# Optimization experiments

Measured on AMD Instinct MI355X. Metric: run time of the kernel, lower is better.

Reference implementation:

```python
import jax, jax.numpy as jnp
import numpy as np

H = 12      # num_heads
EPS = 1e-5  # LayerNorm eps (torch default)


def _ln(x, g, b):
    m = x.mean(-1, keepdims=True)
    v = x.var(-1, keepdims=True)
    return (x - m) * jax.lax.rsqrt(v + EPS) * g + b


def _rot_half(x):
    x1, x2 = x[..., 0::2], x[..., 1::2]
    return jnp.stack((-x2, x1), axis=-1).reshape(x.shape)


def _rope_tables(n, head_dim):
    # rotary-embedding-torch: RotaryEmbedding(dim=head_dim//2, use_xpos=True),
    # theta=10000, scale_base=512. Only first rot=head_dim//2 dims are rotated.
    rot = head_dim // 2
    inv = 1.0 / (10000.0 ** (jnp.arange(0, rot, 2, dtype=jnp.float32) / rot))
    t = jnp.arange(n, dtype=jnp.float32)
    freqs = jnp.repeat(t[:, None] * inv[None, :], 2, axis=-1)  # (n, rot), interleaved
    base = (jnp.arange(0, rot, 2, dtype=jnp.float32) + 0.4 * rot) / (1.4 * rot)
    power = (t - n // 2) / 512.0
    sc = base[None, :] ** power[:, None]
    sc = jnp.concatenate([sc, sc], axis=-1)  # (n, rot), concatenated (library behavior)
    return jnp.cos(freqs), jnp.sin(freqs), sc


def _attn_path(xn, Wqkv, bqkv, Wproj, bproj, qg, qb, kg, kb, R, rg, rb):
    B, N, D = xn.shape
    d = D // H
    qkv = xn @ Wqkv + bqkv
    q, k, v = jnp.split(qkv, 3, axis=-1)
    hd = lambda t: t.reshape(B, N, H, d).transpose(0, 2, 1, 3)  # (B,H,N,d)
    q, k, v = hd(q), hd(k), hd(v)
    q = _ln(q, qg, qb)  # per-head QK LayerNorm
    k = _ln(k, kg, kb)
    cos, sin, sc = _rope_tables(N, d)
    rot = d // 2

    def rope(t, s):  # rotate only first rot dims
        tl, tr = t[..., :rot], t[..., rot:]
        tl = tl * cos * s + _rot_half(tl) * sin * s
        return jnp.concatenate([tl, tr], axis=-1)

    q = rope(q, sc)
    v = rope(v, 1.0 / sc)  # source applies rope to (q, v), not k

    scores = jnp.einsum('bhid,bhjd->bhij', q, k) / jnp.sqrt(jnp.asarray(d, xn.dtype))
    p = jax.nn.softmax(scores, axis=-1)
    # SDPA(q,k,ones_NN)[...,i,j] == sum_k p[...,i,k] for every j (constant over j).
    # All downstream ops (head-mix einsum, LayerNorm over heads, @ v) therefore
    # reduce exactly to the per-(b,i) computation below, avoiding an N^3 matmul.
    s = p.sum(-1)                              # (B,H,N)
    mix = jnp.einsum('bhi,hg->big', s, R)      # (B,N,H)
    w = _ln(mix, rg, rb)                       # reattn LayerNorm over head axis
    vsum = v.sum(axis=2)                       # (B,H,d); (w @ v) with w const over j
    y = jnp.einsum('big,bgd->bigd', w, vsum).reshape(B, N, D)
    return y @ Wproj + bproj


def _cgmlp(xn, W1, b1, gg, gb, cw, cb, W2, b2):
    h = jax.nn.gelu(xn @ W1 + b1, approximate=False)
    c2 = h.shape[-1] // 2
    xr, xg = h[..., :c2], h[..., c2:]
    xg = _ln(xg, gg, gb).transpose(0, 2, 1)  # (B,C,T)
    K = cw.shape[-1]
    xg = jax.lax.conv_general_dilated(xg, cw, (1,), [((K - 1) // 2, (K - 1) // 2)],
                                      dimension_numbers=('NCH', 'OIH', 'NCH'),
                                      feature_group_count=c2)  # depthwise conv1d
    xg = (xg + cb[None, :, None]).transpose(0, 2, 1)
    return (xr * xg) @ W2 + b2


def reference(x, Wqkv, bqkv, Wproj, bproj, qn_g, qn_b, kn_g, kn_b, reattn_w, rn_g, rn_b,
              ln1_g, ln1_b, ln2_g, ln2_b, ls1, ls2, W1, b1, gn_g, gn_b, conv_w, conv_b,
              W2, b2, Wout, bout):
    # eval mode: dropout / drop_path are identity
    xa = _ln(x, ln1_g, ln1_b)
    attn = sum(_attn_path(xa, Wqkv[p], bqkv[p], Wproj[p], bproj[p], qn_g[p], qn_b[p],
                          kn_g[p], kn_b[p], reattn_w[p], rn_g[p], rn_b[p])
               for p in range(2))
    x_attn = x + ls1 * attn
    xm = _ln(x, ln2_g, ln2_b)
    x_mlp = x + ls2 * _cgmlp(xm, W1, b1, gn_g, gn_b, conv_w, conv_b, W2, b2)
    xf = jnp.concatenate([x_attn, x_mlp], axis=-1)
    return xf @ Wout + bout + x


def setup_inputs():
    B, N, D, P = 4, 1024, 768, 2
    d = D // H
    C = 4 * D
    c2 = C // 2
    K = 21
    ks = iter(jax.random.split(jax.random.key(0), 16))
    nrm = lambda s, sd=0.02: jax.random.normal(next(ks), s, jnp.float32) * sd
    return {
        'x': jax.random.normal(next(ks), (B, N, D), jnp.float32),
        'Wqkv': nrm((P, D, 3 * D)), 'bqkv': jnp.zeros((P, 3 * D)),
        'Wproj': nrm((P, D, D)), 'bproj': jnp.zeros((P, D)),
        'qn_g': jnp.ones((P, d)), 'qn_b': jnp.zeros((P, d)),
        'kn_g': jnp.ones((P, d)), 'kn_b': jnp.zeros((P, d)),
        'reattn_w': jax.random.normal(next(ks), (P, H, H), jnp.float32),
        'rn_g': jnp.ones((P, H)), 'rn_b': jnp.zeros((P, H)),
        'ln1_g': jnp.ones((D,)), 'ln1_b': jnp.zeros((D,)),
        'ln2_g': jnp.ones((D,)), 'ln2_b': jnp.zeros((D,)),
        'ls1': jnp.full((D,), 0.01, jnp.float32), 'ls2': jnp.full((D,), 0.01, jnp.float32),
        'W1': nrm((D, C)), 'b1': jnp.zeros((C,)),
        'gn_g': jnp.ones((c2,)), 'gn_b': jnp.zeros((c2,)),
        'conv_w': nrm((c2, 1, K), 0.1), 'conv_b': jnp.zeros((c2,)),
        'W2': nrm((c2, D)), 'b2': jnp.zeros((D,)),
        'Wout': nrm((2 * D, D)), 'bout': jnp.zeros((D,)),
    }
```

## Files before the change

### kernel.cpp

```cpp
#include <hip/hip_runtime.h>
#include <hip/hip_bf16.h>

typedef short s16x8 __attribute__((ext_vector_type(8)));
typedef float f32x4 __attribute__((ext_vector_type(4)));

#define C2 1536

__device__ __forceinline__ float b2f(ushort u){ return __uint_as_float(((unsigned)u)<<16); }
__device__ __forceinline__ ushort f2b(float f){ unsigned u = __float_as_uint(f); return (ushort)((u + 0x7fffu + ((u>>16)&1u)) >> 16); }

#define GL16(g, l) __builtin_amdgcn_global_load_lds( \
    (const __attribute__((address_space(1))) void*)(g), \
    (__attribute__((address_space(3))) void*)(l), 16, 0, 0)

#define VMW(n) asm volatile("s_waitcnt vmcnt(" #n ")" ::: "memory")
#define LGW()  asm volatile("s_waitcnt lgkmcnt(0)" ::: "memory")
#define SB()   __builtin_amdgcn_sched_barrier(0)
#define BAR()  __builtin_amdgcn_s_barrier()
#define SP1    __builtin_amdgcn_s_setprio(1)
#define SP0    __builtin_amdgcn_s_setprio(0)
#define MF(va, vb, c) __builtin_amdgcn_mfma_f32_16x16x32_bf16(va, vb, c, 0,0,0)

#define RDA(P, mh) { const int ab = (P) + aro + (mh)*4096; \
    a0=L8(ab+sx0);      a1=L8(ab+sx1); \
    a2=L8(ab+1024+sx0); a3=L8(ab+1024+sx1); \
    a4=L8(ab+2048+sx0); a5=L8(ab+2048+sx1); \
    a6=L8(ab+3072+sx0); a7=L8(ab+3072+sx1); }
#define RDB0(P, nh) { const int bb = (P) + bro + (nh)*2048; \
    b00=L8(bb+sx0); b01=L8(bb+sx1); b02=L8(bb+1024+sx0); b03=L8(bb+1024+sx1); }
#define RDB1(P, nh) { const int bb = (P) + bro + (nh)*2048; \
    b10=L8(bb+sx0); b11=L8(bb+sx1); b12=L8(bb+1024+sx0); b13=L8(bb+1024+sx1); }
#define L8(off) (*(const s16x8*)&lds[off])
#define STG(p0, p1, T, dstb) { \
    GL16((p0) + (size_t)(T)*64, &lds[(dstb) + ldsw]); \
    GL16((p1) + (size_t)(T)*64, &lds[(dstb) + 4096 + ldsw]); }
#define QD(mh, nh, B0,B1,B2,B3) { \
  acc[(mh)*4+0][(nh)*2+0]=MF(a0,B0,acc[(mh)*4+0][(nh)*2+0]); \
  acc[(mh)*4+0][(nh)*2+0]=MF(a1,B1,acc[(mh)*4+0][(nh)*2+0]); \
  acc[(mh)*4+0][(nh)*2+1]=MF(a0,B2,acc[(mh)*4+0][(nh)*2+1]); \
  acc[(mh)*4+0][(nh)*2+1]=MF(a1,B3,acc[(mh)*4+0][(nh)*2+1]); \
  acc[(mh)*4+1][(nh)*2+0]=MF(a2,B0,acc[(mh)*4+1][(nh)*2+0]); \
  acc[(mh)*4+1][(nh)*2+0]=MF(a3,B1,acc[(mh)*4+1][(nh)*2+0]); \
  acc[(mh)*4+1][(nh)*2+1]=MF(a2,B2,acc[(mh)*4+1][(nh)*2+1]); \
  acc[(mh)*4+1][(nh)*2+1]=MF(a3,B3,acc[(mh)*4+1][(nh)*2+1]); \
  acc[(mh)*4+2][(nh)*2+0]=MF(a4,B0,acc[(mh)*4+2][(nh)*2+0]); \
  acc[(mh)*4+2][(nh)*2+0]=MF(a5,B1,acc[(mh)*4+2][(nh)*2+0]); \
  acc[(mh)*4+2][(nh)*2+1]=MF(a4,B2,acc[(mh)*4+2][(nh)*2+1]); \
  acc[(mh)*4+2][(nh)*2+1]=MF(a5,B3,acc[(mh)*4+2][(nh)*2+1]); \
  acc[(mh)*4+3][(nh)*2+0]=MF(a6,B0,acc[(mh)*4+3][(nh)*2+0]); \
  acc[(mh)*4+3][(nh)*2+0]=MF(a7,B1,acc[(mh)*4+3][(nh)*2+0]); \
  acc[(mh)*4+3][(nh)*2+1]=MF(a6,B2,acc[(mh)*4+3][(nh)*2+1]); \
  acc[(mh)*4+3][(nh)*2+1]=MF(a7,B3,acc[(mh)*4+3][(nh)*2+1]); }

#define EIGHT(t0, t1, DS, VM4) \
   VMW(4); BAR(); \
  RDA(0,0); RDB0(0,0); \
  STG(pA00,pA01,(t1), 16384); \
  LGW(); SB(); SP1; QD(0,0,b00,b01,b02,b03); SP0; BAR(); \
   RDB1(0,1); \
  STG(pA10,pA11,(t1), 24576); \
  BAR(); LGW(); SB(); SP1; QD(0,1,b10,b11,b12,b13); SP0; BAR(); \
   RDA(0,1); \
  if (DS) { STG(pB00,pB01,(t0)+2, 32768); } \
  BAR(); LGW(); SB(); SP1; QD(1,0,b00,b01,b02,b03); SP0; BAR(); \
   if (DS) { STG(pB10,pB11,(t0)+2, 40960); } \
  BAR(); SP1; QD(1,1,b10,b11,b12,b13); SP0; BAR(); \
   VM4; BAR(); \
  RDA(16384,0); RDB0(16384,0); \
  if (DS) { STG(pA00,pA01,(t0)+2, 0); } \
  LGW(); SB(); SP1; QD(0,0,b00,b01,b02,b03); SP0; BAR(); \
   RDB1(16384,1); \
  if (DS) { STG(pA10,pA11,(t0)+2, 8192); } \
  BAR(); LGW(); SB(); SP1; QD(0,1,b10,b11,b12,b13); SP0; BAR(); \
   RDA(16384,1); \
  if (DS) { STG(pB00,pB01,(t1)+2, 49152); } \
  BAR(); LGW(); SB(); SP1; QD(1,0,b00,b01,b02,b03); SP0; BAR(); \
   if (DS) { STG(pB10,pB11,(t1)+2, 57344); } \
  BAR(); SP1; QD(1,1,b10,b11,b12,b13); SP0; BAR();

template<int EPI>
__global__ __launch_bounds__(512, 1) void gemm256(
    const ushort* __restrict__ A, const ushort* __restrict__ BT,
    int M, int N, int K,
    const float* __restrict__ bias,
    ushort* __restrict__ o16, ushort* __restrict__ o16b)
{
    extern __shared__ ushort lds[];
    const int t = threadIdx.x;
    const int lane = t & 63, wv = t >> 6;
    const int wr = wv >> 2, wc = wv & 3;
    const int r0 = lane & 15, q = lane >> 4, e7 = lane & 7;
    const int m0 = blockIdx.y*256, n0 = blockIdx.x*256;

    const int idx = wv*64 + lane;
    const int lr8 = idx >> 3;
    const int ksrc = (idx & 7) ^ (lr8 & 7);
    const ushort* pA00 = A  + (size_t)(m0 +   0 +  0 + lr8)*K + ksrc*8;
    const ushort* pA01 = A  + (size_t)(m0 +   0 + 64 + lr8)*K + ksrc*8;
    const ushort* pA10 = A  + (size_t)(m0 + 128 +  0 + lr8)*K + ksrc*8;
    const ushort* pA11 = A  + (size_t)(m0 + 128 + 64 + lr8)*K + ksrc*8;
    const ushort* pB00 = BT + (size_t)(n0 +   0 +  0 + lr8)*K + ksrc*8;
    const ushort* pB01 = BT + (size_t)(n0 +   0 + 64 + lr8)*K + ksrc*8;
    const ushort* pB10 = BT + (size_t)(n0 + 128 +  0 + lr8)*K + ksrc*8;
    const ushort* pB11 = BT + (size_t)(n0 + 128 + 64 + lr8)*K + ksrc*8;
    const int ldsw = wv*512;

    const int aro = (wr*128 + r0)*64;
    const int bro = 32768 + (wc*64 + r0)*64;
    const int sx0 = (q ^ e7)*8, sx1 = ((q ^ e7)*8) ^ 32;

    f32x4 acc[8][4];
    #pragma unroll
    for (int i=0;i<8;++i)
        #pragma unroll
        for (int j=0;j<4;++j) acc[i][j] = (f32x4){0.f,0.f,0.f,0.f};
    s16x8 a0,a1,a2,a3,a4,a5,a6,a7;
    s16x8 b00,b01,b02,b03, b10,b11,b12,b13;

    const int nkt = K >> 6;
    const int niter = nkt >> 1;

    STG(pB00,pB01, 0, 32768);
    STG(pB10,pB11, 0, 40960);
    STG(pA00,pA01, 0, 0);
    STG(pA10,pA11, 0, 8192);
    STG(pB00,pB01, 1, 49152);
    STG(pB10,pB11, 1, 57344);

    for (int i = 0; i < niter-1; ++i) {
        const int t0 = 2*i, t1 = 2*i+1;
        EIGHT(t0, t1, 1, VMW(4));
    }
    {
        const int t0 = nkt-2, t1 = nkt-1;
        EIGHT(t0, t1, 0, VMW(0));
    }

    #pragma unroll
    for (int gm=0; gm<8; ++gm) {
        #pragma unroll
        for (int gn=0; gn<4; ++gn) {
            int col = n0 + wc*64 + gn*16 + r0;
            #pragma unroll
            for (int r=0; r<4; ++r) {
                int row = m0 + wr*128 + gm*16 + q*4 + r;
                float v = acc[gm][gn][r];
                if (EPI == 0) {
                    o16[(size_t)row*N + col] = f2b(v + bias[col]);
                } else {
                    v += bias[col];
                    float g = 0.5f*v*(1.0f + erff(v*0.70710678118f));
                    if (col < C2) o16 [(size_t)row*C2 + col]        = f2b(g);
                    else          o16b[(size_t)row*C2 + (col - C2)] = f2b(g);
                }
            }
        }
    }
}

template<int EPI>
__global__ __launch_bounds__(256) void gemm_bf16(
    const ushort* __restrict__ A, const ushort* __restrict__ BT,
    int M, int N, int K, int lda, int ldbt,
    const float* __restrict__ bias, const float* __restrict__ xres,
    ushort* __restrict__ o16, float* __restrict__ o32)
{
    __shared__ ushort Al[2][128*32];
    __shared__ ushort Bl[2][128*32];
    const int t = threadIdx.x;
    const int m0 = blockIdx.y*128, n0 = blockIdx.x*128;
    const int lane = t & 63, wv = t >> 6;
    const int wm = (wv>>1)*64, wn = (wv&1)*64;
    const int r0 = lane & 15, q = lane >> 4;

    const int c0i = t, c1i = t + 256;
    const int lrow0 = ((c0i>>6)<<4) | (c0i&15), lkc0 = ((c0i>>4)&3) << 3;
    const int lrow1 = ((c1i>>6)<<4) | (c1i&15), lkc1 = ((c1i>>4)&3) << 3;
    const ushort* gA0 = A  + (size_t)(m0+lrow0)*lda + lkc0;
    const ushort* gB0 = BT + (size_t)(n0+lrow0)*ldbt + lkc0;
    const ushort* gA1 = A  + (size_t)(m0+lrow1)*lda + lkc1;
    const ushort* gB1 = BT + (size_t)(n0+lrow1)*ldbt + lkc1;

    f32x4 acc[4][4];
    #pragma unroll
    for (int i=0;i<4;++i)
        #pragma unroll
        for (int j=0;j<4;++j) acc[i][j] = (f32x4){0.f,0.f,0.f,0.f};

    const int nkt = K >> 5;
    uint4 pa0_0, pb0_0, pa1_0, pb1_0;
    uint4 pa0_1, pb0_1, pa1_1, pb1_1;
    pa0_0 = *(const uint4*)gA0;        pb0_0 = *(const uint4*)gB0;
    pa1_0 = *(const uint4*)gA1;        pb1_0 = *(const uint4*)gB1;
    pa0_1 = *(const uint4*)(gA0 + 32); pb0_1 = *(const uint4*)(gB0 + 32);
    pa1_1 = *(const uint4*)(gA1 + 32); pb1_1 = *(const uint4*)(gB1 + 32);
    *(uint4*)&Al[0][c0i*8] = pa0_0;
    *(uint4*)&Bl[0][c0i*8] = pb0_0;
    *(uint4*)&Al[0][c1i*8] = pa1_0;
    *(uint4*)&Bl[0][c1i*8] = pb1_0;

    for (int kt = 0; kt < nkt; kt += 2) {
        __syncthreads();
        {
            s16x8 af[4], bfr[4];
            #pragma unroll
            for (int mt=0; mt<4; ++mt) af[mt]  = *(const s16x8*)&Al[0][(((wm>>4)+mt)*64 + lane)*8];
            #pragma unroll
            for (int nt=0; nt<4; ++nt) bfr[nt] = *(const s16x8*)&Bl[0][(((wn>>4)+nt)*64 + lane)*8];
            *(uint4*)&Al[1][c0i*8] = pa0_1;
            *(uint4*)&Bl[1][c0i*8] = pb0_1;
            *(uint4*)&Al[1][c1i*8] = pa1_1;
            *(uint4*)&Bl[1][c1i*8] = pb1_1;
            if (kt+2 < nkt) {
                pa0_0 = *(const uint4*)(gA0 + (kt+2)*32);
                pb0_0 = *(const uint4*)(gB0 + (kt+2)*32);
                pa1_0 = *(const uint4*)(gA1 + (kt+2)*32);
                pb1_0 = *(const uint4*)(gB1 + (kt+2)*32);
            }
            #pragma unroll
            for (int mt=0; mt<4; ++mt)
                #pragma unroll
                for (int nt=0; nt<4; ++nt)
                    acc[mt][nt] = __builtin_amdgcn_mfma_f32_16x16x32_bf16(af[mt], bfr[nt], acc[mt][nt], 0,0,0);
        }
        __syncthreads();
        {
            s16x8 af[4], bfr[4];
            #pragma unroll
            for (int mt=0; mt<4; ++mt) af[mt]  = *(const s16x8*)&Al[1][(((wm>>4)+mt)*64 + lane)*8];
            #pragma unroll
            for (int nt=0; nt<4; ++nt) bfr[nt] = *(const s16x8*)&Bl[1][(((wn>>4)+nt)*64 + lane)*8];
            if (kt+2 < nkt) {
                *(uint4*)&Al[0][c0i*8] = pa0_0;
                *(uint4*)&Bl[0][c0i*8] = pb0_0;
                *(uint4*)&Al[0][c1i*8] = pa1_0;
                *(uint4*)&Bl[0][c1i*8] = pb1_0;
            }
            if (kt+3 < nkt) {
                pa0_1 = *(const uint4*)(gA0 + (kt+3)*32);
                pb0_1 = *(const uint4*)(gB0 + (kt+3)*32);
                pa1_1 = *(const uint4*)(gA1 + (kt+3)*32);
                pb1_1 = *(const uint4*)(gB1 + (kt+3)*32);
            }
            #pragma unroll
            for (int mt=0; mt<4; ++mt)
                #pragma unroll
                for (int nt=0; nt<4; ++nt)
                    acc[mt][nt] = __builtin_amdgcn_mfma_f32_16x16x32_bf16(af[mt], bfr[nt], acc[mt][nt], 0,0,0);
        }
    }

    #pragma unroll
    for (int mt=0; mt<4; ++mt) {
        #pragma unroll
        for (int nt=0; nt<4; ++nt) {
            int col = n0 + wn + nt*16 + r0;
            #pragma unroll
            for (int r=0; r<4; ++r) {
                int row = m0 + wm + mt*16 + q*4 + r;
                float v = acc[mt][nt][r];
                if (EPI == 0) {
                    o16[(size_t)row*N + col] = f2b(v + bias[col]);
                } else if (EPI == 3) {
                    o32[(size_t)row*768 + col] = v + bias[(row>>10)*768 + col] + xres[(size_t)row*768 + col];
                } else {
                    o16[(size_t)row*2304 + 768 + col] = f2b(v);
                }
            }
        }
    }
}

__global__ __launch_bounds__(256) void pack_bt(const float* __restrict__ src, ushort* __restrict__ dst,
                                               int K, int ld, int coff)
{
    __shared__ float tl[32*33];
    int kt = blockIdx.x*32, nt = blockIdx.y*32;
    int nl = threadIdx.x & 31, kg = threadIdx.x >> 5;
    #pragma unroll
    for (int kk=0; kk<4; ++kk) {
        int k = kg*4 + kk;
        tl[k*33 + nl] = src[(size_t)(kt + k)*ld + coff + nt + nl];
    }
    __syncthreads();
    int kcol = threadIdx.x & 31, ng = threadIdx.x >> 5;
    #pragma unroll
    for (int nn=0; nn<4; ++nn) {
        int nrow = ng*4 + nn;
        dst[(size_t)(nt + nrow)*K + kt + kcol] = f2b(tl[kcol*33 + nrow]);
    }
}

__global__ __launch_bounds__(256) void pack_bts(const float* __restrict__ src,
    const float* __restrict__ scale, ushort* __restrict__ dst)
{
    __shared__ float tl[32*33];
    int kt = blockIdx.x*32, nt = blockIdx.y*32;
    int nl = threadIdx.x & 31, kg = threadIdx.x >> 5;
    #pragma unroll
    for (int kk=0; kk<4; ++kk) {
        int k = kg*4 + kk;
        tl[k*33 + nl] = src[(size_t)(kt + k)*768 + nt + nl];
    }
    __syncthreads();
    int kcol = threadIdx.x & 31, ng = threadIdx.x >> 5;
    #pragma unroll
    for (int nn=0; nn<4; ++nn) {
        int nrow = ng*4 + nn;
        dst[(size_t)(nt + nrow)*768 + kt + kcol] = f2b(tl[kcol*33 + nrow] * scale[kt + kcol]);
    }
}

__global__ __launch_bounds__(256) void fold1_pack(const float* __restrict__ Wout, ushort* __restrict__ dst)
{
    __shared__ float tl[32*33];
    int kt = blockIdx.x*32, nt = blockIdx.y*32;
    int nl = threadIdx.x & 31, kg = threadIdx.x >> 5;
    #pragma unroll
    for (int kk=0; kk<4; ++kk) {
        int k = kg*4 + kk;
        tl[k*33 + nl] = Wout[(size_t)(kt + k)*768 + nt + nl]
                      + Wout[(size_t)(768 + kt + k)*768 + nt + nl];
    }
    __syncthreads();
    int kcol = threadIdx.x & 31, ng = threadIdx.x >> 5;
    #pragma unroll
    for (int nn=0; nn<4; ++nn) {
        int nrow = ng*4 + nn;
        dst[(size_t)(nt + nrow)*2304 + kt + kcol] = f2b(tl[kcol*33 + nrow]);
    }
}

__global__ __launch_bounds__(256) void cast16(const float* __restrict__ src, ushort* __restrict__ dst, int n)
{
    int i = blockIdx.x*256 + threadIdx.x;
    if (i < n) dst[i] = f2b(src[i]);
}

__global__ __launch_bounds__(256) void pack_bv(const float* __restrict__ bqkv, float* __restrict__ bvp)
{
    int idx = blockIdx.x*256 + threadIdx.x;
    if (idx < 1536) bvp[idx] = bqkv[(idx/768)*2304 + 1536 + (idx%768)];
}

__global__ __launch_bounds__(256) void cvec_kernel(const float* __restrict__ attn_c,
    const float* __restrict__ ls1, const float* __restrict__ ls2, const float* __restrict__ b2,
    const float* __restrict__ Wout, float* __restrict__ cvecb)
{
    int o  = blockIdx.x*256 + threadIdx.x;
    int r0 = blockIdx.y * 96;
    int b  = blockIdx.z;
    float acc = 0.f;
    #pragma unroll 4
    for (int rr = 0; rr < 96; ++rr) {
        int r = r0 + rr;
        float coef = (r < 768) ? ls1[r]*attn_c[b*768 + r]
                               : ls2[r-768]*b2[r-768];
        acc += coef * Wout[(size_t)r*768 + o];
    }
    atomicAdd(&cvecb[b*768 + o], acc);
}

__global__ __launch_bounds__(256) void ln_x_kernel(const float* __restrict__ x,
    const float* __restrict__ g1, const float* __restrict__ b1,
    const float* __restrict__ g2, const float* __restrict__ b2,
    ushort* __restrict__ xa, ushort* __restrict__ xm, ushort* __restrict__ xc)
{
    __shared__ float sb[8];
    int row = blockIdx.x; int t = threadIdx.x;
    float v[3]; float s = 0.f, ss = 0.f;
    #pragma unroll
    for (int e=0; e<3; ++e) { v[e] = x[(size_t)row*768 + t + e*256]; s += v[e]; ss += v[e]*v[e]; }
    for (int o=32; o>0; o>>=1){ s += __shfl_down(s,o,64); ss += __shfl_down(ss,o,64); }
    int lane = t&63, w = t>>6;
    if (lane==0){ sb[w]=s; sb[4+w]=ss; }
    __syncthreads();
    s = sb[0]+sb[1]+sb[2]+sb[3]; ss = sb[4]+sb[5]+sb[6]+sb[7];
    float mean = s*(1.f/768.f);
    float var  = ss*(1.f/768.f) - mean*mean;
    float rstd = rsqrtf(var + 1e-5f);
    #pragma unroll
    for (int e=0; e<3; ++e){
        int c = t + e*256;
        float n = (v[e]-mean)*rstd;
        xa[(size_t)row*768 + c] = f2b(n*g1[c] + b1[c]);
        xm[(size_t)row*768 + c] = f2b(n*g2[c] + b2[c]);
        xc[(size_t)row*2304 + c] = f2b(v[e]);
    }
}

__global__ __launch_bounds__(256) void prep_kernel(
    float* __restrict__ w1t, float* __restrict__ w2t, float* __restrict__ wvec,
    float* __restrict__ attn_c, float* __restrict__ vsum, float* __restrict__ cvecb,
    const float* __restrict__ R, const float* __restrict__ rng,
    const float* __restrict__ rnb, const float* __restrict__ bproj,
    const float* __restrict__ bout)
{
    int idx = blockIdx.x*256 + threadIdx.x;
    {
        int i = idx >> 6, j = idx & 63;
        float w1, w2;
        if (j < 32) {
            int m = j >> 1;
            float inv = powf(10000.f, -(float)m*(1.f/16.f));
            float fr = (float)i * inv;
            float c = cosf(fr), sn = sinf(fr);
            float power = ((float)i - 512.f) * (1.f/512.f);
            float basev = (2.f*(float)(j & 15) + 12.8f) * (1.f/44.8f);
            float sfac = powf(basev, -power);
            w1 = c * sfac;
            w2 = ((j & 1) ? sn : -sn) * sfac;
        } else { w1 = 1.f; w2 = 0.f; }
        w1t[idx] = w1; w2t[idx] = w2;
    }
    if (blockIdx.x >= 1 && blockIdx.x <= 12) {
        int k = (blockIdx.x-1)*256 + threadIdx.x;
        int o = k % 768;
        attn_c[k] = bproj[o] + bproj[768 + o];
    }
    if (blockIdx.x >= 13 && blockIdx.x <= 36) {
        int k = (blockIdx.x-13)*256 + threadIdx.x;
        vsum[k] = 0.f;
    }
    if (blockIdx.x >= 37 && blockIdx.x <= 48) {
        int k = (blockIdx.x-37)*256 + threadIdx.x;
        cvecb[k] = bout[k % 768];
    }
    if (blockIdx.x == 0) {
        __shared__ float mixs[24];
        __shared__ float ws[24];
        int t = threadIdx.x;
        if (t < 24) {
            int p = t / 12, g = t % 12;
            float m = 0.f;
            for (int h=0; h<12; ++h) m += R[p*144 + h*12 + g];
            mixs[t] = m;
        }
        __syncthreads();
        if (t < 2) {
            float mean=0.f, var=0.f;
            for (int g=0; g<12; ++g) mean += mixs[t*12+g];
            mean *= (1.f/12.f);
            for (int g=0; g<12; ++g){ float d = mixs[t*12+g]-mean; var += d*d; }
            var *= (1.f/12.f);
            float rstd = rsqrtf(var + 1e-5f);
            for (int g=0; g<12; ++g)
                ws[t*12+g] = (mixs[t*12+g]-mean)*rstd*rng[t*12+g] + rnb[t*12+g];
        }
        __syncthreads();
        if (t < 24) wvec[t] = ws[t];
    }
}

__global__ __launch_bounds__(256) void rope_reduce(const ushort* __restrict__ V,
    const float* __restrict__ w1t, const float* __restrict__ w2t, float* __restrict__ vsum)
{
    int col = blockIdx.x*256 + threadIdx.x;
    int b = blockIdx.y;
    int i0 = blockIdx.z * 256;
    int j = col & 63;
    float acc = 0.f;
    const ushort* vp = V + (size_t)(b*1024 + i0)*1536;
    #pragma unroll 4
    for (int i=0; i<256; ++i) {
        float v1 = b2f(vp[(size_t)i*1536 + col]);
        float v2 = b2f(vp[(size_t)i*1536 + (col^1)]);
        int ii = i0 + i;
        acc += w1t[ii*64 + j]*v1 + w2t[ii*64 + j]*v2;
    }
    atomicAdd(&vsum[b*1536 + col], acc);
}

__global__ __launch_bounds__(256) void attn_gemm(const float* __restrict__ vsum,
    const float* __restrict__ wvec, const float* __restrict__ Wproj, float* __restrict__ attn_c)
{
    int o  = blockIdx.x*256 + threadIdx.x;
    int c0 = blockIdx.y * 96;
    int b  = blockIdx.z;
    int p  = c0 / 768;
    float acc = 0.f;
    #pragma unroll 4
    for (int cc=0; cc<96; ++cc) {
        int c = c0 + cc;
        int cl = c - p*768;
        float y = wvec[p*12 + (cl>>6)] * vsum[b*1536 + c];
        acc += y * Wproj[(size_t)p*589824 + (size_t)cl*768 + o];
    }
    atomicAdd(&attn_c[b*768 + o], acc);
}

__global__ __launch_bounds__(256) void ln_gate(const ushort* __restrict__ xg,
    const float* __restrict__ g, const float* __restrict__ bta, ushort* __restrict__ out)
{
    __shared__ float sb[8];
    int row = blockIdx.x, t = threadIdx.x;
    float v[6]; float s=0.f, ss=0.f;
    #pragma unroll
    for (int e=0;e<6;++e){ v[e] = b2f(xg[(size_t)row*1536 + t + e*256]); s+=v[e]; ss+=v[e]*v[e]; }
    for (int o=32; o>0; o>>=1){ s += __shfl_down(s,o,64); ss += __shfl_down(ss,o,64); }
    int lane = t&63, w = t>>6;
    if (lane==0){ sb[w]=s; sb[4+w]=ss; }
    __syncthreads();
    s = sb[0]+sb[1]+sb[2]+sb[3]; ss = sb[4]+sb[5]+sb[6]+sb[7];
    float mean = s*(1.f/1536.f);
    float var  = ss*(1.f/1536.f) - mean*mean;
    float rstd = rsqrtf(var + 1e-5f);
    #pragma unroll
    for (int e=0;e<6;++e){
        int c = t + e*256;
        out[(size_t)row*1536 + c] = f2b((v[e]-mean)*rstd*g[c] + bta[c]);
    }
}

#define CROWS 128
#define CIN   (CROWS + 20)
#define CSTR  72
__global__ __launch_bounds__(256) void conv_mul(const ushort* __restrict__ xgln,
    const float* __restrict__ cw, const float* __restrict__ cb,
    const ushort* __restrict__ xr, ushort* __restrict__ u)
{
    __shared__ ushort tile[CIN * CSTR];
    const int c0 = blockIdx.x * 64;
    const int i0 = blockIdx.y * CROWS;
    const int b  = blockIdx.z;
    const int t  = threadIdx.x;
    const size_t base = (size_t)b*1024*1536;

    #pragma unroll
    for (int it = 0; it < 5; ++it) {
        int idx = it*256 + t;
        if (idx < CIN*8) {
            int r  = idx >> 3;
            int cq = (idx & 7) * 8;
            int si = i0 + r - 10;
            uint4 val = make_uint4(0u,0u,0u,0u);
            if (si >= 0 && si < 1024)
                val = *(const uint4*)(xgln + base + (size_t)si*1536 + c0 + cq);
            *(uint4*)&tile[r*CSTR + cq] = val;
        }
    }
    __syncthreads();

    const int ch = t & 63;
    const int o0 = (t >> 6) * 32;
    const int c  = c0 + ch;

    float w[21];
    #pragma unroll
    for (int k=0; k<21; ++k) w[k] = cw[c*21 + k];
    const float bias = cb[c];

    float win[21];
    #pragma unroll
    for (int j=0; j<20; ++j) win[j] = b2f(tile[(o0+j)*CSTR + ch]);

    #pragma unroll
    for (int j=0; j<32; ++j) {
        win[(j+20)%21] = b2f(tile[(o0+j+20)*CSTR + ch]);
        float acc = bias;
        #pragma unroll
        for (int k=0; k<21; ++k) acc += win[(j+k)%21] * w[k];
        size_t offr = base + (size_t)(i0+o0+j)*1536 + c;
        u[(size_t)(b*1024 + i0+o0+j)*2304 + 768 + c] = f2b(b2f(xr[offr]) * acc);
    }
}

extern "C" void kernel_launch(void* const* d_in, const int* in_sizes, int n_in,
                              void* d_out, int out_size, void* d_ws, size_t ws_size,
                              hipStream_t stream)
{
    const float* x     = (const float*)d_in[0];
    const float* Wqkv  = (const float*)d_in[1];
    const float* bqkv  = (const float*)d_in[2];
    const float* Wproj = (const float*)d_in[3];
    const float* bproj = (const float*)d_in[4];
    const float* Rw    = (const float*)d_in[9];
    const float* rng   = (const float*)d_in[10];
    const float* rnb   = (const float*)d_in[11];
    const float* ln1g  = (const float*)d_in[12];
    const float* ln1b  = (const float*)d_in[13];
    const float* ln2g  = (const float*)d_in[14];
    const float* ln2b  = (const float*)d_in[15];
    const float* ls1   = (const float*)d_in[16];
    const float* ls2   = (const float*)d_in[17];
    const float* W1    = (const float*)d_in[18];
    const float* b1    = (const float*)d_in[19];
    const float* gng   = (const float*)d_in[20];
    const float* gnb   = (const float*)d_in[21];
    const float* cw    = (const float*)d_in[22];
    const float* cb    = (const float*)d_in[23];
    const float* W2    = (const float*)d_in[24];
    const float* b2    = (const float*)d_in[25];
    const float* Wout  = (const float*)d_in[26];
    const float* bout  = (const float*)d_in[27];
    float* out = (float*)d_out;

    char* ws = (char*)d_ws;
    size_t off = 0;
    auto alloc = [&](size_t bytes)->char* {
        char* p = ws + off;
        off += (bytes + 255) & ~(size_t)255;
        return p;
    };
    ushort* WvT   = (ushort*)alloc(1536*768*2);
    ushort* W1T   = (ushort*)alloc(3072*768*2);
    ushort* BT2   = (ushort*)alloc(1536*768*2);
    ushort* Afold = (ushort*)alloc(768*768*2);
    ushort* BTf   = (ushort*)alloc(768*2304*2);
    float*  bvp   = (float*)alloc(1536*4);
    float*  w1t   = (float*)alloc(65536*4);
    float*  w2t   = (float*)alloc(65536*4);
    float*  wvec  = (float*)alloc(24*4);
    float*  attnc = (float*)alloc(3072*4);
    float*  vsum  = (float*)alloc(6144*4);
    float*  cvecb = (float*)alloc(3072*4);
    ushort* xa16  = (ushort*)alloc(4096*768*2);
    ushort* xm16  = (ushort*)alloc(4096*768*2);
    ushort* V16   = (ushort*)alloc(4096*1536*2);
    ushort* xg16  = (ushort*)alloc(4096*1536*2);
    ushort* xcat  = (ushort*)alloc((size_t)4096*2304*2);
    ushort* xgln  = xa16;
    ushort* xr16  = V16;
    (void)ws_size; (void)n_in; (void)in_sizes; (void)out_size;

    (void)hipFuncSetAttribute((const void*)gemm256<1>, hipFuncAttributeMaxDynamicSharedMemorySize, 131072);

    for (int p = 0; p < 2; ++p)
        pack_bt<<<dim3(24, 24), 256, 0, stream>>>(Wqkv + (size_t)p*768*2304, WvT + (size_t)p*768*768,
                                                  768, 2304, 1536);
    pack_bt<<<dim3(24, 96), 256, 0, stream>>>(W1, W1T, 768, 3072, 0);
    pack_bv<<<dim3(6), 256, 0, stream>>>(bqkv, bvp);
    prep_kernel<<<dim3(256), 256, 0, stream>>>(w1t, w2t, wvec, attnc, vsum, cvecb,
                                               Rw, rng, rnb, bproj, bout);

    fold1_pack<<<dim3(24, 24), 256, 0, stream>>>(Wout, BTf);
    pack_bts<<<dim3(24, 24), 256, 0, stream>>>(Wout + (size_t)768*768, ls2, Afold);
    cast16<<<dim3(4608), 256, 0, stream>>>(W2, BT2, 1536*768);
    gemm_bf16<4><<<dim3(12, 6), 256, 0, stream>>>(Afold, BT2, 768, 1536, 768, 768, 768,
                                                  nullptr, nullptr, BTf, nullptr);

    ln_x_kernel<<<dim3(4096), 256, 0, stream>>>(x, ln1g, ln1b, ln2g, ln2b, xa16, xm16, xcat);

    gemm_bf16<0><<<dim3(12, 32), 256, 0, stream>>>(xa16, WvT, 4096, 1536, 768, 768, 768,
                                                   bvp, nullptr, V16, nullptr);
    rope_reduce<<<dim3(6, 4, 4), 256, 0, stream>>>(V16, w1t, w2t, vsum);
    attn_gemm<<<dim3(3, 16, 4), 256, 0, stream>>>(vsum, wvec, Wproj, attnc);
    cvec_kernel<<<dim3(3, 16, 4), 256, 0, stream>>>(attnc, ls1, ls2, b2, Wout, cvecb);

    gemm256<1><<<dim3(12, 16), 512, 131072, stream>>>(xm16, W1T, 4096, 3072, 768,
                                                      b1, xr16, xg16);
    ln_gate<<<dim3(4096), 256, 0, stream>>>(xg16, gng, gnb, xgln);
    conv_mul<<<dim3(24, 8, 4), 256, 0, stream>>>(xgln, cw, cb, xr16, xcat);

    gemm_bf16<3><<<dim3(6, 32), 256, 0, stream>>>(xcat, BTf, 4096, 768, 2304, 2304, 2304,
                                                  cvecb, x, nullptr, out);
}
```

Before: 372.7 us.

## Merge weight-packing, prep and input LayerNorm into one launch; split rope reduction finer

Nine small preprocessing kernels (weight transposes and casts, bias packing, rope tables, LayerNorm of x) are merged into a single block-indexed mega_prep kernel, removing launch gaps and letting the independent pieces run concurrently. The rope_reduce grid is also split four times finer along the sequence axis so more blocks share the atomic reduction. In exchange, the single kernel has uneven per-block work and more atomics contend on vsum.

After: 333.8 us. 1.12x faster.

```diff
diff --git a/kernel.cpp b/kernel.cpp
--- a/kernel.cpp
+++ b/kernel.cpp
@@ -271,184 +271,177 @@
     }
 }
 
-__global__ __launch_bounds__(256) void pack_bt(const float* __restrict__ src, ushort* __restrict__ dst,
-                                               int K, int ld, int coff)
-{
-    __shared__ float tl[32*33];
-    int kt = blockIdx.x*32, nt = blockIdx.y*32;
-    int nl = threadIdx.x & 31, kg = threadIdx.x >> 5;
-    #pragma unroll
-    for (int kk=0; kk<4; ++kk) {
-        int k = kg*4 + kk;
-        tl[k*33 + nl] = src[(size_t)(kt + k)*ld + coff + nt + nl];
-    }
-    __syncthreads();
-    int kcol = threadIdx.x & 31, ng = threadIdx.x >> 5;
-    #pragma unroll
-    for (int nn=0; nn<4; ++nn) {
-        int nrow = ng*4 + nn;
-        dst[(size_t)(nt + nrow)*K + kt + kcol] = f2b(tl[kcol*33 + nrow]);
-    }
-}
-
-__global__ __launch_bounds__(256) void pack_bts(const float* __restrict__ src,
-    const float* __restrict__ scale, ushort* __restrict__ dst)
-{
-    __shared__ float tl[32*33];
-    int kt = blockIdx.x*32, nt = blockIdx.y*32;
-    int nl = threadIdx.x & 31, kg = threadIdx.x >> 5;
-    #pragma unroll
-    for (int kk=0; kk<4; ++kk) {
-        int k = kg*4 + kk;
-        tl[k*33 + nl] = src[(size_t)(kt + k)*768 + nt + nl];
-    }
-    __syncthreads();
-    int kcol = threadIdx.x & 31, ng = threadIdx.x >> 5;
-    #pragma unroll
-    for (int nn=0; nn<4; ++nn) {
-        int nrow = ng*4 + nn;
-        dst[(size_t)(nt + nrow)*768 + kt + kcol] = f2b(tl[kcol*33 + nrow] * scale[kt + kcol]);
-    }
-}
-
-__global__ __launch_bounds__(256) void fold1_pack(const float* __restrict__ Wout, ushort* __restrict__ dst)
-{
-    __shared__ float tl[32*33];
-    int kt = blockIdx.x*32, nt = blockIdx.y*32;
-    int nl = threadIdx.x & 31, kg = threadIdx.x >> 5;
-    #pragma unroll
-    for (int kk=0; kk<4; ++kk) {
-        int k = kg*4 + kk;
-        tl[k*33 + nl] = Wout[(size_t)(kt + k)*768 + nt + nl]
-                      + Wout[(size_t)(768 + kt + k)*768 + nt + nl];
-    }
-    __syncthreads();
-    int kcol = threadIdx.x & 31, ng = threadIdx.x >> 5;
-    #pragma unroll
-    for (int nn=0; nn<4; ++nn) {
-        int nrow = ng*4 + nn;
-        dst[(size_t)(nt + nrow)*2304 + kt + kcol] = f2b(tl[kcol*33 + nrow]);
-    }
-}
-
-__global__ __launch_bounds__(256) void cast16(const float* __restrict__ src, ushort* __restrict__ dst, int n)
-{
-    int i = blockIdx.x*256 + threadIdx.x;
-    if (i < n) dst[i] = f2b(src[i]);
-}
-
-__global__ __launch_bounds__(256) void pack_bv(const float* __restrict__ bqkv, float* __restrict__ bvp)
-{
-    int idx = blockIdx.x*256 + threadIdx.x;
-    if (idx < 1536) bvp[idx] = bqkv[(idx/768)*2304 + 1536 + (idx%768)];
-}
-
-__global__ __launch_bounds__(256) void cvec_kernel(const float* __restrict__ attn_c,
-    const float* __restrict__ ls1, const float* __restrict__ ls2, const float* __restrict__ b2,
-    const float* __restrict__ Wout, float* __restrict__ cvecb)
-{
-    int o  = blockIdx.x*256 + threadIdx.x;
-    int r0 = blockIdx.y * 96;
-    int b  = blockIdx.z;
-    float acc = 0.f;
-    #pragma unroll 4
-    for (int rr = 0; rr < 96; ++rr) {
-        int r = r0 + rr;
-        float coef = (r < 768) ? ls1[r]*attn_c[b*768 + r]
-                               : ls2[r-768]*b2[r-768];
-        acc += coef * Wout[(size_t)r*768 + o];
-    }
-    atomicAdd(&cvecb[b*768 + o], acc);
-}
-
-__global__ __launch_bounds__(256) void ln_x_kernel(const float* __restrict__ x,
-    const float* __restrict__ g1, const float* __restrict__ b1,
-    const float* __restrict__ g2, const float* __restrict__ b2,
-    ushort* __restrict__ xa, ushort* __restrict__ xm, ushort* __restrict__ xc)
-{
-    __shared__ float sb[8];
-    int row = blockIdx.x; int t = threadIdx.x;
-    float v[3]; float s = 0.f, ss = 0.f;
-    #pragma unroll
-    for (int e=0; e<3; ++e) { v[e] = x[(size_t)row*768 + t + e*256]; s += v[e]; ss += v[e]*v[e]; }
-    for (int o=32; o>0; o>>=1){ s += __shfl_down(s,o,64); ss += __shfl_down(ss,o,64); }
-    int lane = t&63, w = t>>6;
-    if (lane==0){ sb[w]=s; sb[4+w]=ss; }
-    __syncthreads();
-    s = sb[0]+sb[1]+sb[2]+sb[3]; ss = sb[4]+sb[5]+sb[6]+sb[7];
-    float mean = s*(1.f/768.f);
-    float var  = ss*(1.f/768.f) - mean*mean;
-    float rstd = rsqrtf(var + 1e-5f);
-    #pragma unroll
-    for (int e=0; e<3; ++e){
-        int c = t + e*256;
-        float n = (v[e]-mean)*rstd;
-        xa[(size_t)row*768 + c] = f2b(n*g1[c] + b1[c]);
-        xm[(size_t)row*768 + c] = f2b(n*g2[c] + b2[c]);
-        xc[(size_t)row*2304 + c] = f2b(v[e]);
-    }
-}
-
-__global__ __launch_bounds__(256) void prep_kernel(
+__global__ __launch_bounds__(256) void mega_prep(
+    const float* __restrict__ Wqkv, const float* __restrict__ W1,
+    const float* __restrict__ Wout, const float* __restrict__ W2,
+    const float* __restrict__ ls2,  const float* __restrict__ bqkv,
+    const float* __restrict__ x,
+    const float* __restrict__ g1, const float* __restrict__ b1v,
+    const float* __restrict__ g2, const float* __restrict__ b2v,
+    const float* __restrict__ R,  const float* __restrict__ rng,
+    const float* __restrict__ rnb, const float* __restrict__ bproj,
+    const float* __restrict__ bout,
+    ushort* __restrict__ WvT, ushort* __restrict__ W1T, ushort* __restrict__ BTf,
+    ushort* __restrict__ Afold, ushort* __restrict__ BT2, float* __restrict__ bvp,
     float* __restrict__ w1t, float* __restrict__ w2t, float* __restrict__ wvec,
     float* __restrict__ attn_c, float* __restrict__ vsum, float* __restrict__ cvecb,
-    const float* __restrict__ R, const float* __restrict__ rng,
-    const float* __restrict__ rnb, const float* __restrict__ bproj,
-    const float* __restrict__ bout)
-{
-    int idx = blockIdx.x*256 + threadIdx.x;
-    {
-        int i = idx >> 6, j = idx & 63;
-        float w1, w2;
-        if (j < 32) {
-            int m = j >> 1;
-            float inv = powf(10000.f, -(float)m*(1.f/16.f));
-            float fr = (float)i * inv;
-            float c = cosf(fr), sn = sinf(fr);
-            float power = ((float)i - 512.f) * (1.f/512.f);
-            float basev = (2.f*(float)(j & 15) + 12.8f) * (1.f/44.8f);
-            float sfac = powf(basev, -power);
-            w1 = c * sfac;
-            w2 = ((j & 1) ? sn : -sn) * sfac;
-        } else { w1 = 1.f; w2 = 0.f; }
-        w1t[idx] = w1; w2t[idx] = w2;
-    }
-    if (blockIdx.x >= 1 && blockIdx.x <= 12) {
-        int k = (blockIdx.x-1)*256 + threadIdx.x;
-        int o = k % 768;
-        attn_c[k] = bproj[o] + bproj[768 + o];
-    }
-    if (blockIdx.x >= 13 && blockIdx.x <= 36) {
-        int k = (blockIdx.x-13)*256 + threadIdx.x;
-        vsum[k] = 0.f;
-    }
-    if (blockIdx.x >= 37 && blockIdx.x <= 48) {
-        int k = (blockIdx.x-37)*256 + threadIdx.x;
-        cvecb[k] = bout[k % 768];
-    }
-    if (blockIdx.x == 0) {
-        __shared__ float mixs[24];
-        __shared__ float ws[24];
-        int t = threadIdx.x;
-        if (t < 24) {
-            int p = t / 12, g = t % 12;
-            float m = 0.f;
-            for (int h=0; h<12; ++h) m += R[p*144 + h*12 + g];
-            mixs[t] = m;
+    ushort* __restrict__ xa, ushort* __restrict__ xm, ushort* __restrict__ xc)
+{
+    __shared__ float tl[32*33];
+    const int blk = blockIdx.x;
+    const int t = threadIdx.x;
+
+    if (blk < 1152) {
+        int p = blk / 576, l = blk % 576;
+        int kt = (l % 24)*32, nt = (l / 24)*32;
+        const float* src = Wqkv + (size_t)p*768*2304;
+        ushort* dst = WvT + (size_t)p*768*768;
+        int nl = t & 31, kg = t >> 5;
+        #pragma unroll
+        for (int kk=0; kk<4; ++kk) {
+            int k = kg*4 + kk;
+            tl[k*33 + nl] = src[(size_t)(kt + k)*2304 + 1536 + nt + nl];
         }
         __syncthreads();
-        if (t < 2) {
-            float mean=0.f, var=0.f;
-            for (int g=0; g<12; ++g) mean += mixs[t*12+g];
-            mean *= (1.f/12.f);
-            for (int g=0; g<12; ++g){ float d = mixs[t*12+g]-mean; var += d*d; }
-            var *= (1.f/12.f);
-            float rstd = rsqrtf(var + 1e-5f);
-            for (int g=0; g<12; ++g)
-                ws[t*12+g] = (mixs[t*12+g]-mean)*rstd*rng[t*12+g] + rnb[t*12+g];
+        int kcol = t & 31, ng = t >> 5;
+        #pragma unroll
+        for (int nn=0; nn<4; ++nn) {
+            int nrow = ng*4 + nn;
+            dst[(size_t)(nt + nrow)*768 + kt + kcol] = f2b(tl[kcol*33 + nrow]);
+        }
+    } else if (blk < 3456) {
+        int l = blk - 1152;
+        int kt = (l % 24)*32, nt = (l / 24)*32;
+        int nl = t & 31, kg = t >> 5;
+        #pragma unroll
+        for (int kk=0; kk<4; ++kk) {
+            int k = kg*4 + kk;
+            tl[k*33 + nl] = W1[(size_t)(kt + k)*3072 + nt + nl];
         }
         __syncthreads();
-        if (t < 24) wvec[t] = ws[t];
+        int kcol = t & 31, ng = t >> 5;
+        #pragma unroll
+        for (int nn=0; nn<4; ++nn) {
+            int nrow = ng*4 + nn;
+            W1T[(size_t)(nt + nrow)*768 + kt + kcol] = f2b(tl[kcol*33 + nrow]);
+        }
+    } else if (blk < 4032) {
+        int l = blk - 3456;
+        int kt = (l % 24)*32, nt = (l / 24)*32;
+        int nl = t & 31, kg = t >> 5;
+        #pragma unroll
+        for (int kk=0; kk<4; ++kk) {
+            int k = kg*4 + kk;
+            tl[k*33 + nl] = Wout[(size_t)(kt + k)*768 + nt + nl]
+                          + Wout[(size_t)(768 + kt + k)*768 + nt + nl];
+        }
+        __syncthreads();
+        int kcol = t & 31, ng = t >> 5;
+        #pragma unroll
+        for (int nn=0; nn<4; ++nn) {
+            int nrow = ng*4 + nn;
+            BTf[(size_t)(nt + nrow)*2304 + kt + kcol] = f2b(tl[kcol*33 + nrow]);
+        }
+    } else if (blk < 4608) {
+        int l = blk - 4032;
+        int kt = (l % 24)*32, nt = (l / 24)*32;
+        const float* src = Wout + (size_t)768*768;
+        int nl = t & 31, kg = t >> 5;
+        #pragma unroll
+        for (int kk=0; kk<4; ++kk) {
+            int k = kg*4 + kk;
+            tl[k*33 + nl] = src[(size_t)(kt + k)*768 + nt + nl];
+        }
+        __syncthreads();
+        int kcol = t & 31, ng = t >> 5;
+        #pragma unroll
+        for (int nn=0; nn<4; ++nn) {
+            int nrow = ng*4 + nn;
+            Afold[(size_t)(nt + nrow)*768 + kt + kcol] = f2b(tl[kcol*33 + nrow] * ls2[kt + kcol]);
+        }
+    } else if (blk < 9216) {
+        int i = (blk - 4608)*256 + t;
+        BT2[i] = f2b(W2[i]);
+    } else if (blk < 9222) {
+        int i = (blk - 9216)*256 + t;
+        if (i < 1536) bvp[i] = bqkv[(i/768)*2304 + 1536 + (i%768)];
+    } else if (blk < 9478) {
+        int pb = blk - 9222;
+        int idx = pb*256 + t;
+        {
+            int i = idx >> 6, j = idx & 63;
+            float w1, w2;
+            if (j < 32) {
+                int m = j >> 1;
+                float inv = powf(10000.f, -(float)m*(1.f/16.f));
+                float fr = (float)i * inv;
+                float c = cosf(fr), sn = sinf(fr);
+                float power = ((float)i - 512.f) * (1.f/512.f);
+                float basev = (2.f*(float)(j & 15) + 12.8f) * (1.f/44.8f);
+                float sfac = powf(basev, -power);
+                w1 = c * sfac;
+                w2 = ((j & 1) ? sn : -sn) * sfac;
+            } else { w1 = 1.f; w2 = 0.f; }
+            w1t[idx] = w1; w2t[idx] = w2;
+        }
+        if (pb >= 1 && pb <= 12) {
+            int k = (pb-1)*256 + t;
+            int o = k % 768;
+            attn_c[k] = bproj[o] + bproj[768 + o];
+        }
+        if (pb >= 13 && pb <= 36) {
+            int k = (pb-13)*256 + t;
+            vsum[k] = 0.f;
+        }
+        if (pb >= 37 && pb <= 48) {
+            int k = (pb-37)*256 + t;
+            cvecb[k] = bout[k % 768];
+        }
+        if (pb == 0) {
+            float* mixs = tl;
+            float* wsb  = tl + 32;
+            if (t < 24) {
+                int p = t / 12, g = t % 12;
+                float m = 0.f;
+                for (int h=0; h<12; ++h) m += R[p*144 + h*12 + g];
+                mixs[t] = m;
+            }
+            __syncthreads();
+            if (t < 2) {
+                float mean=0.f, var=0.f;
+                for (int g=0; g<12; ++g) mean += mixs[t*12+g];
+                mean *= (1.f/12.f);
+                for (int g=0; g<12; ++g){ float d = mixs[t*12+g]-mean; var += d*d; }
+                var *= (1.f/12.f);
+                float rstd = rsqrtf(var + 1e-5f);
+                for (int g=0; g<12; ++g)
+                    wsb[t*12+g] = (mixs[t*12+g]-mean)*rstd*rng[t*12+g] + rnb[t*12+g];
+            }
+            __syncthreads();
+            if (t < 24) wvec[t] = wsb[t];
+        }
+    } else {
+        int row = blk - 9478;
+        float* sb = tl;
+        float v[3]; float s = 0.f, ss = 0.f;
+        #pragma unroll
+        for (int e=0; e<3; ++e) { v[e] = x[(size_t)row*768 + t + e*256]; s += v[e]; ss += v[e]*v[e]; }
+        for (int o=32; o>0; o>>=1){ s += __shfl_down(s,o,64); ss += __shfl_down(ss,o,64); }
+        int lane = t&63, w = t>>6;
+        if (lane==0){ sb[w]=s; sb[4+w]=ss; }
+        __syncthreads();
+        s = sb[0]+sb[1]+sb[2]+sb[3]; ss = sb[4]+sb[5]+sb[6]+sb[7];
+        float mean = s*(1.f/768.f);
+        float var  = ss*(1.f/768.f) - mean*mean;
+        float rstd = rsqrtf(var + 1e-5f);
+        #pragma unroll
+        for (int e=0; e<3; ++e){
+            int c = t + e*256;
+            float n = (v[e]-mean)*rstd;
+            xa[(size_t)row*768 + c] = f2b(n*g1[c] + b1v[c]);
+            xm[(size_t)row*768 + c] = f2b(n*g2[c] + b2v[c]);
+            xc[(size_t)row*2304 + c] = f2b(v[e]);
+        }
     }
 }
 
@@ -457,12 +450,12 @@
 {
     int col = blockIdx.x*256 + threadIdx.x;
     int b = blockIdx.y;
-    int i0 = blockIdx.z * 256;
+    int i0 = blockIdx.z * 64;
     int j = col & 63;
     float acc = 0.f;
     const ushort* vp = V + (size_t)(b*1024 + i0)*1536;
     #pragma unroll 4
-    for (int i=0; i<256; ++i) {
+    for (int i=0; i<64; ++i) {
         float v1 = b2f(vp[(size_t)i*1536 + col]);
         float v2 = b2f(vp[(size_t)i*1536 + (col^1)]);
         int ii = i0 + i;
@@ -487,6 +480,24 @@
         acc += y * Wproj[(size_t)p*589824 + (size_t)cl*768 + o];
     }
     atomicAdd(&attn_c[b*768 + o], acc);
+}
+
+__global__ __launch_bounds__(256) void cvec_kernel(const float* __restrict__ attn_c,
+    const float* __restrict__ ls1, const float* __restrict__ ls2, const float* __restrict__ b2,
+    const float* __restrict__ Wout, float* __restrict__ cvecb)
+{
+    int o  = blockIdx.x*256 + threadIdx.x;
+    int r0 = blockIdx.y * 96;
+    int b  = blockIdx.z;
+    float acc = 0.f;
+    #pragma unroll 4
+    for (int rr = 0; rr < 96; ++rr) {
+        int r = r0 + rr;
+        float coef = (r < 768) ? ls1[r]*attn_c[b*768 + r]
+                               : ls2[r-768]*b2[r-768];
+        acc += coef * Wout[(size_t)r*768 + o];
+    }
+    atomicAdd(&cvecb[b*768 + o], acc);
 }
 
 __global__ __launch_bounds__(256) void ln_gate(const ushort* __restrict__ xg,
@@ -625,25 +636,19 @@
 
     (void)hipFuncSetAttribute((const void*)gemm256<1>, hipFuncAttributeMaxDynamicSharedMemorySize, 131072);
 
-    for (int p = 0; p < 2; ++p)
-        pack_bt<<<dim3(24, 24), 256, 0, stream>>>(Wqkv + (size_t)p*768*2304, WvT + (size_t)p*768*768,
-                                                  768, 2304, 1536);
-    pack_bt<<<dim3(24, 96), 256, 0, stream>>>(W1, W1T, 768, 3072, 0);
-    pack_bv<<<dim3(6), 256, 0, stream>>>(bqkv, bvp);
-    prep_kernel<<<dim3(256), 256, 0, stream>>>(w1t, w2t, wvec, attnc, vsum, cvecb,
-                                               Rw, rng, rnb, bproj, bout);
-
-    fold1_pack<<<dim3(24, 24), 256, 0, stream>>>(Wout, BTf);
-    pack_bts<<<dim3(24, 24), 256, 0, stream>>>(Wout + (size_t)768*768, ls2, Afold);
-    cast16<<<dim3(4608), 256, 0, stream>>>(W2, BT2, 1536*768);
+    mega_prep<<<dim3(13574), 256, 0, stream>>>(
+        Wqkv, W1, Wout, W2, ls2, bqkv, x,
+        ln1g, ln1b, ln2g, ln2b, Rw, rng, rnb, bproj, bout,
+        WvT, W1T, BTf, Afold, BT2, bvp,
+        w1t, w2t, wvec, attnc, vsum, cvecb,
+        xa16, xm16, xcat);
+
     gemm_bf16<4><<<dim3(12, 6), 256, 0, stream>>>(Afold, BT2, 768, 1536, 768, 768, 768,
                                                   nullptr, nullptr, BTf, nullptr);
 
-    ln_x_kernel<<<dim3(4096), 256, 0, stream>>>(x, ln1g, ln1b, ln2g, ln2b, xa16, xm16, xcat);
-
     gemm_bf16<0><<<dim3(12, 32), 256, 0, stream>>>(xa16, WvT, 4096, 1536, 768, 768, 768,
                                                    bvp, nullptr, V16, nullptr);
-    rope_reduce<<<dim3(6, 4, 4), 256, 0, stream>>>(V16, w1t, w2t, vsum);
+    rope_reduce<<<dim3(6, 4, 16), 256, 0, stream>>>(V16, w1t, w2t, vsum);
     attn_gemm<<<dim3(3, 16, 4), 256, 0, stream>>>(vsum, wvec, Wproj, attnc);
     cvec_kernel<<<dim3(3, 16, 4), 256, 0, stream>>>(attnc, ls1, ls2, b2, Wout, cvecb);
 
```
